# Optimization experiments

Measured on AMD Instinct MI355X. Metric: run time of the kernel, lower is better.

## Reference

```python
import jax, jax.numpy as jnp
import numpy as np

NUM_INPUTS = 376
NUM_ACTIONS = 17
L1, L2 = 256, 128
BHID = 128
NE = 2
B = 65536


def setup_inputs() -> dict:
    key = jax.random.key(0)
    ks = jax.random.split(key, 16)
    s = lambda k, shape: jax.random.normal(k, shape, dtype=jnp.float32) * 0.05
    return {
        "states": jax.random.normal(ks[0], (B, NUM_INPUTS), dtype=jnp.float32),
        # blending module params
        "bw1": s(ks[1], (BHID, NUM_INPUTS)), "bb1": s(ks[2], (BHID,)),
        "bw2": s(ks[3], (BHID, BHID)),       "bb2": s(ks[4], (BHID,)),
        "bwo": s(ks[5], (NE, BHID)),         "bbo": s(ks[6], (NE,)),
        # stacked expert (p1, p2) policy params, leading axis = expert
        "ew1": s(ks[7], (NE, L1, NUM_INPUTS)), "eb1": s(ks[8], (NE, L1)),
        "ew2": s(ks[9], (NE, L2, L1)),         "eb2": s(ks[10], (NE, L2)),
        "ewm": s(ks[11], (NE, NUM_ACTIONS, L2)), "ebm": s(ks[12], (NE, NUM_ACTIONS)),
    }


def _blended_linear(h, coeffs, W, b):
    # Linear with per-sample blended weights: (sum_e c_e W_e) h + sum_e c_e b_e
    # == sum_e c_e (W_e h + b_e), so compute both expert outputs and blend.
    y = jnp.einsum('bi,eoi->beo', h, W) + b[None]  # [B, E, O]
    return jnp.einsum('be,beo->bo', coeffs, y)


def reference(states, bw1, bb1, bw2, bb2, bwo, bbo, ew1, eb1, ew2, eb2, ewm, ebm):
    # BlendingModule: 2-layer relu MLP -> softmax over experts
    g = jax.nn.relu(states @ bw1.T + bb1)
    g = jax.nn.relu(g @ bw2.T + bb2)
    coeffs = jax.nn.softmax(g @ bwo.T + bbo, axis=-1)  # [B, 2]
    # Per-sample blended PolicyModule (256 -> 128 -> actions, tanh head)
    h = jax.nn.relu(_blended_linear(states, coeffs, ew1, eb1))
    h = jax.nn.relu(_blended_linear(h, coeffs, ew2, eb2))
    mu = jnp.tanh(_blended_linear(h, coeffs, ewm, ebm))
    return mu
```

## Files before the change

kernel.cpp:

```cpp
#include <hip/hip_runtime.h>
#include <math.h>


typedef __attribute__((ext_vector_type(8))) _Float16 half8;
typedef __attribute__((ext_vector_type(4))) _Float16 half4;
typedef __attribute__((ext_vector_type(4))) float    f32x4;

#define MFMA16(a, b, c) __builtin_amdgcn_mfma_f32_16x16x32_f16((a), (b), (c), 0, 0, 0)
#define SWZ(row) (((row) & 7) << 4)

#define MT 32
#define T  512

#define S_B      0
#define G1_B     24576
#define G2_B     32768
#define H1_B     24576
#define H2_B     24576
#define CF_B     40960
#define LDS_BYTES 41216

#define WS_W1 0
#define WS_W2 49152
#define WS_E1 65536
#define WS_E2 262144
#define WS_EM 327680
#define WS_HALFS 335872
#define WS_BYTES 671744

__device__ __forceinline__ half8 cvt8(const float* __restrict__ p) {
    const float4 a = *reinterpret_cast<const float4*>(p);
    const float4 b = *reinterpret_cast<const float4*>(p + 4);
    half8 r;
    r[0] = (_Float16)a.x; r[1] = (_Float16)a.y; r[2] = (_Float16)a.z; r[3] = (_Float16)a.w;
    r[4] = (_Float16)b.x; r[5] = (_Float16)b.y; r[6] = (_Float16)b.z; r[7] = (_Float16)b.w;
    return r;
}

__global__ __launch_bounds__(256)
void prep_weights(const float* __restrict__ bw1, const float* __restrict__ bb1,
                  const float* __restrict__ bw2,
                  const float* __restrict__ ew1, const float* __restrict__ eb1,
                  const float* __restrict__ ew2,
                  const float* __restrict__ ewm, _Float16* __restrict__ wsw)
{
    const int i = blockIdx.x * 256 + threadIdx.x;
    if (i >= WS_HALFS) return;
    int sec; const float* W; const float* Bv; int N, K, KC, j0;
    if      (i < 49152)  { sec = 0; W = bw1; Bv = bb1;    N = 128; K = 376; KC = 12; j0 = i - WS_W1; }
    else if (i < 65536)  { sec = 1; W = bw2; Bv = nullptr; N = 128; K = 128; KC = 4;  j0 = i - WS_W2; }
    else if (i < 262144) { sec = 2; W = ew1; Bv = eb1;    N = 512; K = 376; KC = 12; j0 = i - WS_E1; }
    else if (i < 327680) { sec = 3; W = ew2; Bv = nullptr; N = 256; K = 256; KC = 8;  j0 = i - WS_E2; }
    else                 { sec = 4; W = ewm; Bv = nullptr; N = 34;  K = 128; KC = 4;  j0 = i - WS_EM; }
    const int tile = j0 >> 9;
    const int rem  = j0 & 511;
    const int l    = rem >> 3;
    const int jj   = rem & 7;
    const int n0   = tile / KC, kc = tile - n0 * KC;
    const int n = n0 * 16 + (l & 15);
    const int k = kc * 32 + (l >> 4) * 8 + jj;
    float v = 0.f;
    if (sec == 4) {
        const int e = n >> 5, a = n & 31;
        if (a < 17 && k < K) v = ewm[(e * 17 + a) * K + k];
    } else if (n < N) {
        if (k < K)                 v = W[n * K + k];
        else if (k == K && Bv)     v = Bv[n];
    }
    wsw[i] = (_Float16)v;
}

template <bool USE_WS>
__global__ __launch_bounds__(512)
__attribute__((amdgpu_waves_per_eu(2)))
void actor_kernel(const float* __restrict__ states,
                  const float* __restrict__ bw1, const float* __restrict__ bb1,
                  const float* __restrict__ bw2, const float* __restrict__ bb2,
                  const float* __restrict__ bwo, const float* __restrict__ bbo,
                  const float* __restrict__ ew1, const float* __restrict__ eb1,
                  const float* __restrict__ ew2, const float* __restrict__ eb2,
                  const float* __restrict__ ewm, const float* __restrict__ ebm,
                  const _Float16* __restrict__ wsw,
                  float* __restrict__ out)
{
    extern __shared__ char smc[];
    const int t    = threadIdx.x;
    const int l    = t & 63;
    const int l15  = l & 15;
    const int kgrp = l >> 4;
    const int kg16 = kgrp * 16;
    const int wv   = __builtin_amdgcn_readfirstlane(t >> 6);
    const int base = blockIdx.x * MT;
    const int lB   = l * 8;

    const half8 zf = {0,0,0,0,0,0,0,0};

    {
        const float4* src = reinterpret_cast<const float4*>(states + (long)base * 376);
        for (int q = t; q < MT * 94; q += T) {
            const int r  = q / 94;
            const int c4 = q - r * 94;
            const float4 v = src[q];
            half4 h;
            h[0] = (_Float16)v.x; h[1] = (_Float16)v.y;
            h[2] = (_Float16)v.z; h[3] = (_Float16)v.w;
            *(half4*)(smc + S_B + ((r * 768 + c4 * 8) ^ SWZ(r))) = h;
        }
        if (t < MT) {
            const int off = (t * 768 + 752) ^ SWZ(t);
            *(ushort4*)(smc + S_B + off)     = make_ushort4(0x3C00u, 0, 0, 0);
            *(ushort4*)(smc + S_B + off + 8) = make_ushort4(0, 0, 0, 0);
        }
    }
    __syncthreads();

    {
        f32x4 acc[2] = {{0,0,0,0},{0,0,0,0}};
        const int col = wv * 16 + l15;
        auto ldW = [&](int kc) -> half8 {
            if constexpr (USE_WS) return *(const half8*)(wsw + WS_W1 + (wv * 12 + kc) * 512 + lB);
            else {
                const int g = kc * 4 + kgrp;
                if (g < 47) return cvt8(bw1 + col * 376 + g * 8);
                half8 rr = zf; rr[0] = (_Float16)bb1[col]; return rr;
            }
        };
        half8 bf = ldW(0);
        #pragma unroll
        for (int kc = 0; kc < 12; ++kc) {
            const half8 cur = bf;
            if (kc < 11) bf = ldW(kc + 1);
            const int koff = kc * 64 + kg16;
            #pragma unroll
            for (int mt = 0; mt < 2; ++mt) {
                const int row = mt * 16 + l15;
                const half8 af = *(const half8*)(smc + S_B + ((row * 768 + koff) ^ SWZ(row)));
                acc[mt] = MFMA16(af, cur, acc[mt]);
            }
        }
        #pragma unroll
        for (int mt = 0; mt < 2; ++mt) {
            #pragma unroll
            for (int j = 0; j < 4; ++j) {
                const int row = mt * 16 + kgrp * 4 + j;
                const float v = fmaxf(acc[mt][j], 0.f);
                *(_Float16*)(smc + G1_B + ((row * 256 + col * 2) ^ SWZ(row))) = (_Float16)v;
            }
        }
    }
    __syncthreads();

    {
        f32x4 acc[2] = {{0,0,0,0},{0,0,0,0}};
        const int col = wv * 16 + l15;
        auto ldW = [&](int kc) -> half8 {
            if constexpr (USE_WS) return *(const half8*)(wsw + WS_W2 + (wv * 4 + kc) * 512 + lB);
            else                  return cvt8(bw2 + col * 128 + (kc * 4 + kgrp) * 8);
        };
        half8 bf = ldW(0);
        #pragma unroll
        for (int kc = 0; kc < 4; ++kc) {
            const half8 cur = bf;
            if (kc < 3) bf = ldW(kc + 1);
            const int koff = kc * 64 + kg16;
            #pragma unroll
            for (int mt = 0; mt < 2; ++mt) {
                const int row = mt * 16 + l15;
                const half8 af = *(const half8*)(smc + G1_B + ((row * 256 + koff) ^ SWZ(row)));
                acc[mt] = MFMA16(af, cur, acc[mt]);
            }
        }
        const float bias = bb2[col];
        #pragma unroll
        for (int mt = 0; mt < 2; ++mt) {
            #pragma unroll
            for (int j = 0; j < 4; ++j) {
                const int row = mt * 16 + kgrp * 4 + j;
                const float v = fmaxf(acc[mt][j] + bias, 0.f);
                *(_Float16*)(smc + G2_B + ((row * 256 + col * 2) ^ SWZ(row))) = (_Float16)v;
            }
        }
    }
    __syncthreads();

    {
        const int s     = t >> 4;
        const int r     = t & 15;
        const int e     = r & 1;
        const int chunk = r >> 1;
        float z = 0.f;
        const float* wo = bwo + e * 128 + chunk * 16;
        #pragma unroll
        for (int q = 0; q < 2; ++q) {
            const half8 hv = *(const half8*)(smc + G2_B + ((s * 256 + chunk * 32 + q * 16) ^ SWZ(s)));
            const float4 w0 = *(const float4*)(wo + q * 8);
            const float4 w1 = *(const float4*)(wo + q * 8 + 4);
            z = fmaf((float)hv[0], w0.x, z); z = fmaf((float)hv[1], w0.y, z);
            z = fmaf((float)hv[2], w0.z, z); z = fmaf((float)hv[3], w0.w, z);
            z = fmaf((float)hv[4], w1.x, z); z = fmaf((float)hv[5], w1.y, z);
            z = fmaf((float)hv[6], w1.z, z); z = fmaf((float)hv[7], w1.w, z);
        }
        z += __shfl_xor(z, 2, 64);
        z += __shfl_xor(z, 4, 64);
        z += __shfl_xor(z, 8, 64);
        z += bbo[e];
        const float zo = __shfl_xor(z, 1, 64);
        if (r < 2) {
            const float m = fmaxf(z, zo);
            const float ea = __expf(z - m), eb = __expf(zo - m);
            *(float*)(smc + CF_B + s * 8 + e * 4) = ea / (ea + eb);
        }
    }
    __syncthreads();

    {
        f32x4 aA[2][2], aB[2][2];
        #pragma unroll
        for (int nt = 0; nt < 2; ++nt)
            #pragma unroll
            for (int mt = 0; mt < 2; ++mt) { aA[nt][mt] = {0,0,0,0}; aB[nt][mt] = {0,0,0,0}; }

        auto ldE1 = [&](int kc, int nt, int ex) -> half8 {
            if constexpr (USE_WS) {
                const int n0 = wv * 2 + nt + ex * 16;
                return *(const half8*)(wsw + WS_E1 + (n0 * 12 + kc) * 512 + lB);
            } else {
                const int g = kc * 4 + kgrp;
                const int wr = wv * 32 + nt * 16 + l15 + ex * 256;
                if (g < 47) return cvt8(ew1 + wr * 376 + g * 8);
                half8 rr = zf; rr[0] = (_Float16)eb1[wr]; return rr;
            }
        };
        half8 b00 = ldE1(0, 0, 0), b01 = ldE1(0, 0, 1);
        half8 b10 = ldE1(0, 1, 0), b11 = ldE1(0, 1, 1);
        #pragma unroll
        for (int kc = 0; kc < 12; ++kc) {
            const half8 c00 = b00, c01 = b01, c10 = b10, c11 = b11;
            if (kc < 11) {
                b00 = ldE1(kc + 1, 0, 0); b01 = ldE1(kc + 1, 0, 1);
                b10 = ldE1(kc + 1, 1, 0); b11 = ldE1(kc + 1, 1, 1);
            }
            const int koff = kc * 64 + kg16;
            #pragma unroll
            for (int mt = 0; mt < 2; ++mt) {
                const int row = mt * 16 + l15;
                const half8 af = *(const half8*)(smc + S_B + ((row * 768 + koff) ^ SWZ(row)));
                aA[0][mt] = MFMA16(af, c00, aA[0][mt]);
                aB[0][mt] = MFMA16(af, c01, aB[0][mt]);
                aA[1][mt] = MFMA16(af, c10, aA[1][mt]);
                aB[1][mt] = MFMA16(af, c11, aB[1][mt]);
            }
        }
        #pragma unroll
        for (int nt = 0; nt < 2; ++nt) {
            const int col = wv * 32 + nt * 16 + l15;
            #pragma unroll
            for (int mt = 0; mt < 2; ++mt) {
                #pragma unroll
                for (int j = 0; j < 4; ++j) {
                    const int row = mt * 16 + kgrp * 4 + j;
                    const float2 cc = *(const float2*)(smc + CF_B + row * 8);
                    const float v = fmaxf(cc.x * aA[nt][mt][j] + cc.y * aB[nt][mt][j], 0.f);
                    *(_Float16*)(smc + H1_B + ((row * 512 + col * 2) ^ SWZ(row))) = (_Float16)v;
                }
            }
        }
    }
    __syncthreads();

    {
        f32x4 cA[2], cB[2];
        #pragma unroll
        for (int mt = 0; mt < 2; ++mt) { cA[mt] = {0,0,0,0}; cB[mt] = {0,0,0,0}; }
        const int col = wv * 16 + l15;
        auto ldE2 = [&](int kc, int ex) -> half8 {
            if constexpr (USE_WS) {
                return *(const half8*)(wsw + WS_E2 + ((wv + ex * 8) * 8 + kc) * 512 + lB);
            } else {
                const int g = kc * 4 + kgrp;
                return cvt8(ew2 + (col + ex * 128) * 256 + g * 8);
            }
        };
        half8 b0 = ldE2(0, 0), b1 = ldE2(0, 1);
        #pragma unroll
        for (int kc = 0; kc < 8; ++kc) {
            const half8 c0f = b0, c1f = b1;
            if (kc < 7) { b0 = ldE2(kc + 1, 0); b1 = ldE2(kc + 1, 1); }
            const int koff = kc * 64 + kg16;
            #pragma unroll
            for (int mt = 0; mt < 2; ++mt) {
                const int row = mt * 16 + l15;
                const half8 af = *(const half8*)(smc + H1_B + ((row * 512 + koff) ^ SWZ(row)));
                cA[mt] = MFMA16(af, c0f, cA[mt]);
                cB[mt] = MFMA16(af, c1f, cB[mt]);
            }
        }
        __syncthreads();
        const float b0s = eb2[col], b1s = eb2[128 + col];
        #pragma unroll
        for (int mt = 0; mt < 2; ++mt) {
            #pragma unroll
            for (int j = 0; j < 4; ++j) {
                const int row = mt * 16 + kgrp * 4 + j;
                const float2 cc = *(const float2*)(smc + CF_B + row * 8);
                const float v = fmaxf(cc.x * (cA[mt][j] + b0s) + cc.y * (cB[mt][j] + b1s), 0.f);
                *(_Float16*)(smc + H2_B + ((row * 256 + col * 2) ^ SWZ(row))) = (_Float16)v;
            }
        }
    }
    __syncthreads();

    if (wv < 4) {
        const int colt = wv & 1;
        const int mt   = wv >> 1;
        f32x4 c0a = {0,0,0,0}, c1a = {0,0,0,0};
        const int col  = colt * 16 + l15;
        const bool vcol = (col < 17);
        const int arow = mt * 16 + l15;
        for (int kc = 0; kc < 4; ++kc) {
            const int koff = kc * 64 + kg16;
            const half8 af = *(const half8*)(smc + H2_B + ((arow * 256 + koff) ^ SWZ(arow)));
            half8 b0, b1;
            if constexpr (USE_WS) {
                b0 = *(const half8*)(wsw + WS_EM + (colt * 4 + kc) * 512 + lB);
                b1 = *(const half8*)(wsw + WS_EM + ((2 + colt) * 4 + kc) * 512 + lB);
            } else {
                const int g = kc * 4 + kgrp;
                b0 = vcol ? cvt8(ewm + col * 128 + g * 8)        : zf;
                b1 = vcol ? cvt8(ewm + (17 + col) * 128 + g * 8) : zf;
            }
            c0a = MFMA16(af, b0, c0a);
            c1a = MFMA16(af, b1, c1a);
        }
        if (vcol) {
            const float b0 = ebm[col], b1 = ebm[17 + col];
            #pragma unroll
            for (int j = 0; j < 4; ++j) {
                const int row = mt * 16 + kgrp * 4 + j;
                const float2 cc = *(const float2*)(smc + CF_B + row * 8);
                const float z = cc.x * (c0a[j] + b0) + cc.y * (c1a[j] + b1);
                const float e2x = __expf(2.f * z);
                out[(long)(base + row) * 17 + col] = 1.f - 2.f / (e2x + 1.f);
            }
        }
    }
}

extern "C" void kernel_launch(void* const* d_in, const int* in_sizes, int n_in,
                              void* d_out, int out_size, void* d_ws, size_t ws_size,
                              hipStream_t stream) {
    (void)in_sizes; (void)n_in; (void)out_size;
    const float* states = (const float*)d_in[0];
    const float* bw1 = (const float*)d_in[1];
    const float* bb1 = (const float*)d_in[2];
    const float* bw2 = (const float*)d_in[3];
    const float* bb2 = (const float*)d_in[4];
    const float* bwo = (const float*)d_in[5];
    const float* bbo = (const float*)d_in[6];
    const float* ew1 = (const float*)d_in[7];
    const float* eb1 = (const float*)d_in[8];
    const float* ew2 = (const float*)d_in[9];
    const float* eb2 = (const float*)d_in[10];
    const float* ewm = (const float*)d_in[11];
    const float* ebm = (const float*)d_in[12];
    float* out = (float*)d_out;

    const int nblk = 65536 / MT;

    if (d_ws != nullptr && ws_size >= (size_t)WS_BYTES) {
        _Float16* wsw = (_Float16*)d_ws;
        prep_weights<<<dim3((WS_HALFS + 255) / 256), dim3(256), 0, stream>>>(
            bw1, bb1, bw2, ew1, eb1, ew2, ewm, wsw);
        actor_kernel<true><<<dim3(nblk), dim3(T), LDS_BYTES, stream>>>(
            states, bw1, bb1, bw2, bb2, bwo, bbo,
            ew1, eb1, ew2, eb2, ewm, ebm, wsw, out);
    } else {
        actor_kernel<false><<<dim3(nblk), dim3(T), LDS_BYTES, stream>>>(
            states, bw1, bb1, bw2, bb2, bwo, bbo,
            ew1, eb1, ew2, eb2, ewm, ebm, nullptr, out);
    }
}
```

Baseline: 84.45 us.

## Double per-block row tile to 64 and pack blend coefficients into states padding

Raises the number of batch rows per block from 32 to 64, so each weight fragment loaded from global memory feeds four MFMA row tiles instead of two. To fit in LDS, the gating buffers are merged, and the softmax coefficients are stored as hi/lo fp16 pairs in the unused padding of the states tile rather than in a separate buffer. The expert layer-1 loop now runs over its two column tiles in sequence, and all eight waves take part in the final action head. In exchange, LDS use roughly doubles and register pressure rises, which may cut occupancy, and the block count halves.

```diff
diff --git a/kernel.cpp b/kernel.cpp
--- a/kernel.cpp
+++ b/kernel.cpp
@@ -9,16 +9,14 @@
 #define MFMA16(a, b, c) __builtin_amdgcn_mfma_f32_16x16x32_f16((a), (b), (c), 0, 0, 0)
 #define SWZ(row) (((row) & 7) << 4)
 
-#define MT 32
+#define MT 64
 #define T  512
 
-#define S_B      0
-#define G1_B     24576
-#define G2_B     32768
-#define H1_B     24576
-#define H2_B     24576
-#define CF_B     40960
-#define LDS_BYTES 41216
+#define S_B   0
+#define G_B   49152
+#define H1_B  49152
+#define H2_B  49152
+#define LDS_BYTES 81920
 
 #define WS_W1 0
 #define WS_W2 49152
@@ -47,9 +45,9 @@
     const int i = blockIdx.x * 256 + threadIdx.x;
     if (i >= WS_HALFS) return;
     int sec; const float* W; const float* Bv; int N, K, KC, j0;
-    if      (i < 49152)  { sec = 0; W = bw1; Bv = bb1;    N = 128; K = 376; KC = 12; j0 = i - WS_W1; }
+    if      (i < 49152)  { sec = 0; W = bw1; Bv = bb1;     N = 128; K = 376; KC = 12; j0 = i - WS_W1; }
     else if (i < 65536)  { sec = 1; W = bw2; Bv = nullptr; N = 128; K = 128; KC = 4;  j0 = i - WS_W2; }
-    else if (i < 262144) { sec = 2; W = ew1; Bv = eb1;    N = 512; K = 376; KC = 12; j0 = i - WS_E1; }
+    else if (i < 262144) { sec = 2; W = ew1; Bv = eb1;     N = 512; K = 376; KC = 12; j0 = i - WS_E1; }
     else if (i < 327680) { sec = 3; W = ew2; Bv = nullptr; N = 256; K = 256; KC = 8;  j0 = i - WS_E2; }
     else                 { sec = 4; W = ewm; Bv = nullptr; N = 34;  K = 128; KC = 4;  j0 = i - WS_EM; }
     const int tile = j0 >> 9;
@@ -64,8 +62,8 @@
         const int e = n >> 5, a = n & 31;
         if (a < 17 && k < K) v = ewm[(e * 17 + a) * K + k];
     } else if (n < N) {
-        if (k < K)                 v = W[n * K + k];
-        else if (k == K && Bv)     v = Bv[n];
+        if (k < K)             v = W[n * K + k];
+        else if (k == K && Bv) v = Bv[n];
     }
     wsw[i] = (_Float16)v;
 }
@@ -115,7 +113,7 @@
     __syncthreads();
 
     {
-        f32x4 acc[2] = {{0,0,0,0},{0,0,0,0}};
+        f32x4 acc[4] = {{0,0,0,0},{0,0,0,0},{0,0,0,0},{0,0,0,0}};
         const int col = wv * 16 + l15;
         auto ldW = [&](int kc) -> half8 {
             if constexpr (USE_WS) return *(const half8*)(wsw + WS_W1 + (wv * 12 + kc) * 512 + lB);
@@ -132,26 +130,26 @@
             if (kc < 11) bf = ldW(kc + 1);
             const int koff = kc * 64 + kg16;
             #pragma unroll
-            for (int mt = 0; mt < 2; ++mt) {
+            for (int mt = 0; mt < 4; ++mt) {
                 const int row = mt * 16 + l15;
                 const half8 af = *(const half8*)(smc + S_B + ((row * 768 + koff) ^ SWZ(row)));
                 acc[mt] = MFMA16(af, cur, acc[mt]);
             }
         }
         #pragma unroll
-        for (int mt = 0; mt < 2; ++mt) {
+        for (int mt = 0; mt < 4; ++mt) {
             #pragma unroll
             for (int j = 0; j < 4; ++j) {
                 const int row = mt * 16 + kgrp * 4 + j;
                 const float v = fmaxf(acc[mt][j], 0.f);
-                *(_Float16*)(smc + G1_B + ((row * 256 + col * 2) ^ SWZ(row))) = (_Float16)v;
-            }
-        }
-    }
-    __syncthreads();
-
-    {
-        f32x4 acc[2] = {{0,0,0,0},{0,0,0,0}};
+                *(_Float16*)(smc + G_B + ((row * 256 + col * 2) ^ SWZ(row))) = (_Float16)v;
+            }
+        }
+    }
+    __syncthreads();
+
+    {
+        f32x4 acc[4] = {{0,0,0,0},{0,0,0,0},{0,0,0,0},{0,0,0,0}};
         const int col = wv * 16 + l15;
         auto ldW = [&](int kc) -> half8 {
             if constexpr (USE_WS) return *(const half8*)(wsw + WS_W2 + (wv * 4 + kc) * 512 + lB);
@@ -164,35 +162,36 @@
             if (kc < 3) bf = ldW(kc + 1);
             const int koff = kc * 64 + kg16;
             #pragma unroll
-            for (int mt = 0; mt < 2; ++mt) {
+            for (int mt = 0; mt < 4; ++mt) {
                 const int row = mt * 16 + l15;
-                const half8 af = *(const half8*)(smc + G1_B + ((row * 256 + koff) ^ SWZ(row)));
+                const half8 af = *(const half8*)(smc + G_B + ((row * 256 + koff) ^ SWZ(row)));
                 acc[mt] = MFMA16(af, cur, acc[mt]);
             }
         }
+        __syncthreads();
         const float bias = bb2[col];
         #pragma unroll
-        for (int mt = 0; mt < 2; ++mt) {
+        for (int mt = 0; mt < 4; ++mt) {
             #pragma unroll
             for (int j = 0; j < 4; ++j) {
                 const int row = mt * 16 + kgrp * 4 + j;
                 const float v = fmaxf(acc[mt][j] + bias, 0.f);
-                *(_Float16*)(smc + G2_B + ((row * 256 + col * 2) ^ SWZ(row))) = (_Float16)v;
-            }
-        }
-    }
-    __syncthreads();
-
-    {
-        const int s     = t >> 4;
-        const int r     = t & 15;
+                *(_Float16*)(smc + G_B + ((row * 256 + col * 2) ^ SWZ(row))) = (_Float16)v;
+            }
+        }
+    }
+    __syncthreads();
+
+    {
+        const int s     = t >> 3;
+        const int r     = t & 7;
         const int e     = r & 1;
         const int chunk = r >> 1;
         float z = 0.f;
-        const float* wo = bwo + e * 128 + chunk * 16;
-        #pragma unroll
-        for (int q = 0; q < 2; ++q) {
-            const half8 hv = *(const half8*)(smc + G2_B + ((s * 256 + chunk * 32 + q * 16) ^ SWZ(s)));
+        const float* wo = bwo + e * 128 + chunk * 32;
+        #pragma unroll
+        for (int q = 0; q < 4; ++q) {
+            const half8 hv = *(const half8*)(smc + G_B + ((s * 256 + chunk * 64 + q * 16) ^ SWZ(s)));
             const float4 w0 = *(const float4*)(wo + q * 8);
             const float4 w1 = *(const float4*)(wo + q * 8 + 4);
             z = fmaf((float)hv[0], w0.x, z); z = fmaf((float)hv[1], w0.y, z);
@@ -202,76 +201,71 @@
         }
         z += __shfl_xor(z, 2, 64);
         z += __shfl_xor(z, 4, 64);
-        z += __shfl_xor(z, 8, 64);
         z += bbo[e];
         const float zo = __shfl_xor(z, 1, 64);
         if (r < 2) {
             const float m = fmaxf(z, zo);
             const float ea = __expf(z - m), eb = __expf(zo - m);
-            *(float*)(smc + CF_B + s * 8 + e * 4) = ea / (ea + eb);
-        }
-    }
-    __syncthreads();
-
-    {
-        f32x4 aA[2][2], aB[2][2];
-        #pragma unroll
-        for (int nt = 0; nt < 2; ++nt)
-            #pragma unroll
-            for (int mt = 0; mt < 2; ++mt) { aA[nt][mt] = {0,0,0,0}; aB[nt][mt] = {0,0,0,0}; }
-
-        auto ldE1 = [&](int kc, int nt, int ex) -> half8 {
+            const float c_self = ea / (ea + eb);
+            const _Float16 ch = (_Float16)c_self;
+            const _Float16 cl = (_Float16)(c_self - (float)ch);
+            union { _Float16 h[2]; unsigned u; } pk;
+            pk.h[0] = ch; pk.h[1] = cl;
+            *(unsigned*)(smc + S_B + (((s * 768 + 752) ^ SWZ(s)) + 8 + e * 4)) = pk.u;
+        }
+    }
+    __syncthreads();
+
+    #pragma unroll
+    for (int p = 0; p < 2; ++p) {
+        f32x4 aA[4], aB[4];
+        #pragma unroll
+        for (int mt = 0; mt < 4; ++mt) { aA[mt] = {0,0,0,0}; aB[mt] = {0,0,0,0}; }
+        auto ldE1 = [&](int kc, int ex) -> half8 {
             if constexpr (USE_WS) {
-                const int n0 = wv * 2 + nt + ex * 16;
+                const int n0 = wv * 2 + p + ex * 16;
                 return *(const half8*)(wsw + WS_E1 + (n0 * 12 + kc) * 512 + lB);
             } else {
                 const int g = kc * 4 + kgrp;
-                const int wr = wv * 32 + nt * 16 + l15 + ex * 256;
+                const int wr = wv * 32 + p * 16 + l15 + ex * 256;
                 if (g < 47) return cvt8(ew1 + wr * 376 + g * 8);
                 half8 rr = zf; rr[0] = (_Float16)eb1[wr]; return rr;
             }
         };
-        half8 b00 = ldE1(0, 0, 0), b01 = ldE1(0, 0, 1);
-        half8 b10 = ldE1(0, 1, 0), b11 = ldE1(0, 1, 1);
+        half8 b0 = ldE1(0, 0), b1 = ldE1(0, 1);
         #pragma unroll
         for (int kc = 0; kc < 12; ++kc) {
-            const half8 c00 = b00, c01 = b01, c10 = b10, c11 = b11;
-            if (kc < 11) {
-                b00 = ldE1(kc + 1, 0, 0); b01 = ldE1(kc + 1, 0, 1);
-                b10 = ldE1(kc + 1, 1, 0); b11 = ldE1(kc + 1, 1, 1);
-            }
-            const int koff = kc * 64 + kg16;
-            #pragma unroll
-            for (int mt = 0; mt < 2; ++mt) {
+            const half8 c0f = b0, c1f = b1;
+            if (kc < 11) { b0 = ldE1(kc + 1, 0); b1 = ldE1(kc + 1, 1); }
+            const int koff = kc * 64 + kg16;
+            #pragma unroll
+            for (int mt = 0; mt < 4; ++mt) {
                 const int row = mt * 16 + l15;
                 const half8 af = *(const half8*)(smc + S_B + ((row * 768 + koff) ^ SWZ(row)));
-                aA[0][mt] = MFMA16(af, c00, aA[0][mt]);
-                aB[0][mt] = MFMA16(af, c01, aB[0][mt]);
-                aA[1][mt] = MFMA16(af, c10, aA[1][mt]);
-                aB[1][mt] = MFMA16(af, c11, aB[1][mt]);
-            }
-        }
-        #pragma unroll
-        for (int nt = 0; nt < 2; ++nt) {
-            const int col = wv * 32 + nt * 16 + l15;
-            #pragma unroll
-            for (int mt = 0; mt < 2; ++mt) {
-                #pragma unroll
-                for (int j = 0; j < 4; ++j) {
-                    const int row = mt * 16 + kgrp * 4 + j;
-                    const float2 cc = *(const float2*)(smc + CF_B + row * 8);
-                    const float v = fmaxf(cc.x * aA[nt][mt][j] + cc.y * aB[nt][mt][j], 0.f);
-                    *(_Float16*)(smc + H1_B + ((row * 512 + col * 2) ^ SWZ(row))) = (_Float16)v;
-                }
-            }
-        }
-    }
-    __syncthreads();
-
-    {
-        f32x4 cA[2], cB[2];
-        #pragma unroll
-        for (int mt = 0; mt < 2; ++mt) { cA[mt] = {0,0,0,0}; cB[mt] = {0,0,0,0}; }
+                aA[mt] = MFMA16(af, c0f, aA[mt]);
+                aB[mt] = MFMA16(af, c1f, aB[mt]);
+            }
+        }
+        const int col = wv * 32 + p * 16 + l15;
+        #pragma unroll
+        for (int mt = 0; mt < 4; ++mt) {
+            #pragma unroll
+            for (int j = 0; j < 4; ++j) {
+                const int row = mt * 16 + kgrp * 4 + j;
+                const half4 cc = *(const half4*)(smc + S_B + (((row * 768 + 752) ^ SWZ(row)) + 8));
+                const float c0 = (float)cc[0] + (float)cc[1];
+                const float c1 = (float)cc[2] + (float)cc[3];
+                const float v = fmaxf(c0 * aA[mt][j] + c1 * aB[mt][j], 0.f);
+                *(_Float16*)(smc + H1_B + ((row * 512 + col * 2) ^ SWZ(row))) = (_Float16)v;
+            }
+        }
+    }
+    __syncthreads();
+
+    {
+        f32x4 cA[4], cB[4];
+        #pragma unroll
+        for (int mt = 0; mt < 4; ++mt) { cA[mt] = {0,0,0,0}; cB[mt] = {0,0,0,0}; }
         const int col = wv * 16 + l15;
         auto ldE2 = [&](int kc, int ex) -> half8 {
             if constexpr (USE_WS) {
@@ -288,7 +282,7 @@
             if (kc < 7) { b0 = ldE2(kc + 1, 0); b1 = ldE2(kc + 1, 1); }
             const int koff = kc * 64 + kg16;
             #pragma unroll
-            for (int mt = 0; mt < 2; ++mt) {
+            for (int mt = 0; mt < 4; ++mt) {
                 const int row = mt * 16 + l15;
                 const half8 af = *(const half8*)(smc + H1_B + ((row * 512 + koff) ^ SWZ(row)));
                 cA[mt] = MFMA16(af, c0f, cA[mt]);
@@ -298,25 +292,27 @@
         __syncthreads();
         const float b0s = eb2[col], b1s = eb2[128 + col];
         #pragma unroll
-        for (int mt = 0; mt < 2; ++mt) {
+        for (int mt = 0; mt < 4; ++mt) {
             #pragma unroll
             for (int j = 0; j < 4; ++j) {
                 const int row = mt * 16 + kgrp * 4 + j;
-                const float2 cc = *(const float2*)(smc + CF_B + row * 8);
-                const float v = fmaxf(cc.x * (cA[mt][j] + b0s) + cc.y * (cB[mt][j] + b1s), 0.f);
+                const half4 cc = *(const half4*)(smc + S_B + (((row * 768 + 752) ^ SWZ(row)) + 8));
+                const float c0 = (float)cc[0] + (float)cc[1];
+                const float c1 = (float)cc[2] + (float)cc[3];
+                const float v = fmaxf(c0 * (cA[mt][j] + b0s) + c1 * (cB[mt][j] + b1s), 0.f);
                 *(_Float16*)(smc + H2_B + ((row * 256 + col * 2) ^ SWZ(row))) = (_Float16)v;
             }
         }
     }
     __syncthreads();
 
-    if (wv < 4) {
+    {
         const int colt = wv & 1;
-        const int mt   = wv >> 1;
+        const int mtq  = wv >> 1;
         f32x4 c0a = {0,0,0,0}, c1a = {0,0,0,0};
         const int col  = colt * 16 + l15;
         const bool vcol = (col < 17);
-        const int arow = mt * 16 + l15;
+        const int arow = mtq * 16 + l15;
         for (int kc = 0; kc < 4; ++kc) {
             const int koff = kc * 64 + kg16;
             const half8 af = *(const half8*)(smc + H2_B + ((arow * 256 + koff) ^ SWZ(arow)));
@@ -336,9 +332,11 @@
             const float b0 = ebm[col], b1 = ebm[17 + col];
             #pragma unroll
             for (int j = 0; j < 4; ++j) {
-                const int row = mt * 16 + kgrp * 4 + j;
-                const float2 cc = *(const float2*)(smc + CF_B + row * 8);
-                const float z = cc.x * (c0a[j] + b0) + cc.y * (c1a[j] + b1);
+                const int row = mtq * 16 + kgrp * 4 + j;
+                const half4 cc = *(const half4*)(smc + S_B + (((row * 768 + 752) ^ SWZ(row)) + 8));
+                const float c0 = (float)cc[0] + (float)cc[1];
+                const float c1 = (float)cc[2] + (float)cc[3];
+                const float z = c0 * (c0a[j] + b0) + c1 * (c1a[j] + b1);
                 const float e2x = __expf(2.f * z);
                 out[(long)(base + row) * 17 + col] = 1.f - 2.f / (e2x + 1.f);
             }
```

After: 98.12 us. 1.16x slower.
